# Kernel tuning notes

Measured on AMD Instinct MI355X. Metric: run time of the kernel, lower is better.

## Reference

```python
import jax, jax.numpy as jnp
import numpy as np

N, E, G = 50000, 800000, 512
C = 128          # in_channels = hidden_out_channel = out_channel
K = 3            # Chebyshev order (nb_filters)
NUM_EMB = 119    # largest OGB atom feature cardinality (padded common table)
EPS = 1e-5


def setup_inputs() -> dict:
    key = jax.random.key(0)
    ks = jax.random.split(key, 12)
    s = 0.05
    return {
        "atom_emb": jax.random.normal(ks[0], (9, NUM_EMB, C), jnp.float32) * s,
        "W1": jax.random.normal(ks[1], (K, C, C), jnp.float32) * s,
        "b1": jnp.zeros((C,), jnp.float32),
        "W3": jax.random.normal(ks[2], (K, C, C), jnp.float32) * s,
        "b3": jnp.zeros((C,), jnp.float32),
        "gamma": jnp.ones((C,), jnp.float32),
        "beta": jnp.zeros((C,), jnp.float32),
        "lw1": jax.random.normal(ks[3], (C, 16), jnp.float32) * s,
        "lb1": jnp.zeros((16,), jnp.float32),
        "lw2": jax.random.normal(ks[4], (16, 2), jnp.float32) * s,
        "lb2": jnp.zeros((2,), jnp.float32),
        "x": jax.random.randint(ks[5], (N, 9), 0, 2),
        "edge_index": jax.random.randint(ks[6], (2, E), 0, N),
        "batch": jnp.sort(jax.random.randint(ks[7], (N,), 0, G)),
    }


def _cheb_conv(h, row, col, norm, W, b):
    # PyG ChebConv, sym norm, lambda_max=2 => Lhat = -D^{-1/2} A D^{-1/2} (zero diag)
    def Lhat(z):
        return jax.ops.segment_sum(norm[:, None] * z[col], row, num_segments=N)
    Tx1 = Lhat(h)                      # T_1 = Lhat x
    Tx2 = 2.0 * Lhat(Tx1) - h          # T_2 = 2 Lhat T_1 - T_0
    return h @ W[0] + Tx1 @ W[1] + Tx2 @ W[2] + b


def reference(atom_emb, W1, b1, W3, b3, gamma, beta, lw1, lb1, lw2, lb2,
              x, edge_index, batch):
    row, col = edge_index[0], edge_index[1]
    # symmetric normalization weights (deg computed on row, as in get_laplacian)
    deg = jax.ops.segment_sum(jnp.ones((E,), jnp.float32), row, num_segments=N)
    dis = jnp.where(deg > 0, jax.lax.rsqrt(jnp.maximum(deg, 1.0)), 0.0)
    norm = -(dis[row] * dis[col])      # [E]

    # AtomEncoder: sum of 9 per-feature embeddings -> [N, C]
    h = atom_emb[jnp.arange(9), x].sum(axis=1)

    h = jax.nn.relu(_cheb_conv(h, row, col, norm, W1, b1))   # conv1
    h = jax.nn.relu(_cheb_conv(h, row, col, norm, W3, b3))   # conv3 (conv2 unused)

    # BatchNorm over nodes (training-mode batch stats, biased var)
    mu = h.mean(axis=0)
    var = jnp.mean((h - mu) ** 2, axis=0)
    h = (h - mu) * jax.lax.rsqrt(var + EPS) * gamma + beta

    # global_mean_pool over graphs
    sums = jax.ops.segment_sum(h, batch, num_segments=G)
    cnt = jax.ops.segment_sum(jnp.ones((N,), jnp.float32), batch, num_segments=G)
    pooled = sums / jnp.maximum(cnt, 1.0)[:, None]           # [G, C]

    out = jax.nn.relu(pooled @ lw1 + lb1) @ lw2 + lb2        # [G, 2]
    return out
```

## Files before the change

kernel.cpp:

```cpp
#include <hip/hip_runtime.h>
#include <hip/hip_bf16.h>

typedef __hip_bfloat16 bf16;
#define BN_EPS 1e-5f

typedef __attribute__((ext_vector_type(8))) short bf16x8;
typedef __attribute__((ext_vector_type(4))) float f32x4;

__device__ __forceinline__ float b2f(bf16 v){ return __bfloat162float(v); }
__device__ __forceinline__ float bu2f(unsigned short u){
  union { unsigned int i; float f; } x; x.i = ((unsigned int)u) << 16; return x.f;
}
__device__ __forceinline__ unsigned short f2bu(float f){
  bf16 b = __float2bfloat16(f);
  union { bf16 b; unsigned short u; } x; x.b = b; return x.u;
}
__device__ __forceinline__ float ldw(const void* p, size_t i, int wf){
  return wf ? ((const float*)p)[i] : b2f(((const bf16*)p)[i]);
}
__device__ __forceinline__ void up2(unsigned int w, float& lo, float& hi){
  union { unsigned int i; float f; } L, H;
  L.i = w << 16; H.i = w & 0xffff0000u;
  lo = L.f; hi = H.f;
}

__global__ void k_zero(int* __restrict__ p, int n,
                       const unsigned int* __restrict__ gbits, int* __restrict__ flag){
  int i = blockIdx.x * blockDim.x + threadIdx.x;
  if (i == 0) *flag = (gbits[0] == 0x3F800000u) ? 1 : 0;
  if (i < n) p[i] = 0;
}

__global__ __launch_bounds__(256) void k_bhist(const int* __restrict__ row, int E,
                                               int* __restrict__ gcnt){
  __shared__ int hist[256];
  int t = threadIdx.x;
  hist[t] = 0;
  __syncthreads();
  int base = blockIdx.x * 4096;
  #pragma unroll
  for (int j = 0; j < 16; ++j){
    int e = base + (j << 8) + t;
    if (e < E) atomicAdd(&hist[row[e] >> 8], 1);
  }
  __syncthreads();
  int h = hist[t];
  if (h > 0) atomicAdd(&gcnt[t], h);
}

__global__ __launch_bounds__(256) void k_bbase(const int* __restrict__ gcnt,
    int* __restrict__ bucketBase, int* __restrict__ gcur, int* __restrict__ rp, int N){
  __shared__ int ss[256];
  int t = threadIdx.x;
  int v = gcnt[t];
  ss[t] = v; __syncthreads();
  for (int o = 1; o < 256; o <<= 1){
    int u = (t >= o) ? ss[t - o] : 0;
    __syncthreads();
    ss[t] += u;
    __syncthreads();
  }
  int ex = ss[t] - v;
  bucketBase[t] = ex;
  gcur[t] = ex;
  if (t == 255){ bucketBase[256] = ss[255]; rp[N] = ss[255]; }
}

__global__ __launch_bounds__(256) void k_prep(int N,
    const void* __restrict__ Wa, unsigned short* __restrict__ WTa,
    const void* __restrict__ Wb, unsigned short* __restrict__ WTb,
    const void* __restrict__ emb, const int* __restrict__ x, int NE,
    unsigned short* __restrict__ h, const int* __restrict__ flag){
  int b = blockIdx.x;
  int t = threadIdx.x;
  int wf = *flag;
  if (b < 384){
    int id = b * 256 + t;
    const void* W = (id < 49152) ? Wa : Wb;
    unsigned short* WT = (id < 49152) ? WTa : WTb;
    int i = (id < 49152) ? id : id - 49152;
    int r = i >> 7, n = i & 127;
    float v;
    if (r < 128)       v = ldw(W, (size_t)r * 128 + n, wf)
                         - ldw(W, ((size_t)(256 + r)) * 128 + n, wf);
    else if (r < 256)  v = ldw(W, (size_t)r * 128 + n, wf);
    else               v = 2.f * ldw(W, (size_t)r * 128 + n, wf);
    WT[(size_t)n * 384 + r] = f2bu(v);
    return;
  }
  int gid = (b - 384) * 256 + t;
  int n = gid >> 4, c8 = (gid & 15) << 3;
  if (n >= N) return;
  float s[8];
  #pragma unroll
  for (int j = 0; j < 8; ++j) s[j] = 0.f;
  #pragma unroll
  for (int f = 0; f < 9; ++f){
    int idx = x[n * 9 + f];
    size_t base = ((size_t)(f * NE + idx) << 7) + c8;
    if (wf){
      const float* ep = (const float*)emb + base;
      #pragma unroll
      for (int j = 0; j < 8; ++j) s[j] += ep[j];
    } else {
      uint4 v = *(const uint4*)((const unsigned short*)emb + base);
      float lo, hi;
      up2(v.x, lo, hi); s[0] += lo; s[1] += hi;
      up2(v.y, lo, hi); s[2] += lo; s[3] += hi;
      up2(v.z, lo, hi); s[4] += lo; s[5] += hi;
      up2(v.w, lo, hi); s[6] += lo; s[7] += hi;
    }
  }
  uint4 r;
  r.x = ((unsigned int)f2bu(s[1]) << 16) | f2bu(s[0]);
  r.y = ((unsigned int)f2bu(s[3]) << 16) | f2bu(s[2]);
  r.z = ((unsigned int)f2bu(s[5]) << 16) | f2bu(s[4]);
  r.w = ((unsigned int)f2bu(s[7]) << 16) | f2bu(s[6]);
  *(uint4*)(h + ((size_t)n << 7) + c8) = r;
}

__global__ __launch_bounds__(256) void k_bfill1(const int* __restrict__ row,
    const int* __restrict__ col, int E,
    int* __restrict__ gcur, unsigned int* __restrict__ ebuf){
  __shared__ int hist[256];
  __shared__ int curs[256];
  int t = threadIdx.x;
  hist[t] = 0;
  __syncthreads();
  int base = blockIdx.x * 4096;
  int r[16], c[16];
  #pragma unroll
  for (int j = 0; j < 16; ++j){
    int e = base + (j << 8) + t;
    if (e < E){
      r[j] = row[e]; c[j] = col[e];
      atomicAdd(&hist[r[j] >> 8], 1);
    } else r[j] = -1;
  }
  __syncthreads();
  int h = hist[t];
  if (h > 0) curs[t] = atomicAdd(&gcur[t], h);
  __syncthreads();
  #pragma unroll
  for (int j = 0; j < 16; ++j){
    if (r[j] >= 0){
      int p = atomicAdd(&curs[r[j] >> 8], 1);
      ebuf[p] = ((unsigned int)c[j] << 8) | ((unsigned int)r[j] & 255u);
    }
  }
}

__global__ __launch_bounds__(256) void k_bfill2a(const unsigned int* __restrict__ ebuf,
    const int* __restrict__ bucketBase, int N,
    int* __restrict__ rp, float* __restrict__ dis){
  __shared__ int cnt[256];
  __shared__ int ss[256];
  int b = blockIdx.x, t = threadIdx.x;
  cnt[t] = 0;
  __syncthreads();
  int beg = bucketBase[b], end = bucketBase[b + 1];
  for (int p = beg + t; p < end; p += 256)
    atomicAdd(&cnt[ebuf[p] & 255u], 1);
  __syncthreads();
  int v = cnt[t];
  ss[t] = v; __syncthreads();
  for (int o = 1; o < 256; o <<= 1){
    int u = (t >= o) ? ss[t - o] : 0;
    __syncthreads();
    ss[t] += u;
    __syncthreads();
  }
  int idx = (b << 8) + t;
  if (idx < N){
    rp[idx] = beg + ss[t] - v;
    dis[idx] = (v > 0) ? rsqrtf((float)v) : 0.f;
  }
}

__global__ __launch_bounds__(256) void k_bfill2b(const unsigned int* __restrict__ ebuf,
    const int* __restrict__ bucketBase, const int* __restrict__ rp, int N,
    const float* __restrict__ dis, int2* __restrict__ cpack){
  __shared__ int lcur[256];
  __shared__ float sdis[256];
  int b = blockIdx.x, t = threadIdx.x;
  int idx = (b << 8) + t;
  lcur[t] = (idx < N) ? rp[idx] : 0;
  sdis[t] = (idx < N) ? dis[idx] : 0.f;
  __syncthreads();
  int beg = bucketBase[b], end = bucketBase[b + 1];
  for (int p = beg + t; p < end; p += 256){
    unsigned int pw = ebuf[p];
    int c = (int)(pw >> 8);
    int rl = (int)(pw & 255u);
    float nm = -(sdis[rl] * dis[c]);
    int slot = atomicAdd(&lcur[rl], 1);
    cpack[slot] = make_int2(c, __float_as_int(nm));
  }
}

__global__ __launch_bounds__(256) void k_spmm(const unsigned short* __restrict__ in,
    const int* __restrict__ rp, const int2* __restrict__ cpack,
    unsigned short* __restrict__ out, int N){
  int w = (blockIdx.x * 256 + threadIdx.x) >> 6;
  if (w >= N) return;
  int lane = threadIdx.x & 63;
  int quad = lane >> 4, ql = lane & 15;
  int p1 = rp[w + 1];
  int p = rp[w] + quad;
  const unsigned short* inq = in + (ql << 3);
  float a0 = 0.f, a1 = 0.f, a2 = 0.f, a3 = 0.f;
  float a4 = 0.f, a5 = 0.f, a6 = 0.f, a7 = 0.f;
  for (; p + 4 < p1; p += 8){
    int2 e0 = cpack[p];
    int2 e1 = cpack[p + 4];
    uint4 v0 = *(const uint4*)(inq + ((size_t)e0.x << 7));
    uint4 v1 = *(const uint4*)(inq + ((size_t)e1.x << 7));
    float w0 = __int_as_float(e0.y);
    float w1 = __int_as_float(e1.y);
    float lo, hi;
    up2(v0.x, lo, hi); a0 += w0 * lo; a1 += w0 * hi;
    up2(v0.y, lo, hi); a2 += w0 * lo; a3 += w0 * hi;
    up2(v0.z, lo, hi); a4 += w0 * lo; a5 += w0 * hi;
    up2(v0.w, lo, hi); a6 += w0 * lo; a7 += w0 * hi;
    up2(v1.x, lo, hi); a0 += w1 * lo; a1 += w1 * hi;
    up2(v1.y, lo, hi); a2 += w1 * lo; a3 += w1 * hi;
    up2(v1.z, lo, hi); a4 += w1 * lo; a5 += w1 * hi;
    up2(v1.w, lo, hi); a6 += w1 * lo; a7 += w1 * hi;
  }
  if (p < p1){
    int2 e0 = cpack[p];
    uint4 v0 = *(const uint4*)(inq + ((size_t)e0.x << 7));
    float w0 = __int_as_float(e0.y);
    float lo, hi;
    up2(v0.x, lo, hi); a0 += w0 * lo; a1 += w0 * hi;
    up2(v0.y, lo, hi); a2 += w0 * lo; a3 += w0 * hi;
    up2(v0.z, lo, hi); a4 += w0 * lo; a5 += w0 * hi;
    up2(v0.w, lo, hi); a6 += w0 * lo; a7 += w0 * hi;
  }
  a0 += __shfl_xor(a0, 16); a0 += __shfl_xor(a0, 32);
  a1 += __shfl_xor(a1, 16); a1 += __shfl_xor(a1, 32);
  a2 += __shfl_xor(a2, 16); a2 += __shfl_xor(a2, 32);
  a3 += __shfl_xor(a3, 16); a3 += __shfl_xor(a3, 32);
  a4 += __shfl_xor(a4, 16); a4 += __shfl_xor(a4, 32);
  a5 += __shfl_xor(a5, 16); a5 += __shfl_xor(a5, 32);
  a6 += __shfl_xor(a6, 16); a6 += __shfl_xor(a6, 32);
  a7 += __shfl_xor(a7, 16); a7 += __shfl_xor(a7, 32);
  if (quad == 0){
    uint4 r;
    r.x = ((unsigned int)f2bu(a1) << 16) | f2bu(a0);
    r.y = ((unsigned int)f2bu(a3) << 16) | f2bu(a2);
    r.z = ((unsigned int)f2bu(a5) << 16) | f2bu(a4);
    r.w = ((unsigned int)f2bu(a7) << 16) | f2bu(a6);
    *(uint4*)(out + ((size_t)w << 7) + (ql << 3)) = r;
  }
}

__global__ __launch_bounds__(256) void k_conv(const unsigned short* __restrict__ X,
    const unsigned short* __restrict__ T1, const unsigned short* __restrict__ T2,
    const unsigned short* __restrict__ WT,
    const void* __restrict__ bias,
    unsigned short* __restrict__ Y, int N, const int* __restrict__ flag,
    float* __restrict__ bns){
  int wf = *flag;
  __shared__ unsigned short As[128 * 40];
  __shared__ unsigned short Ws[128 * 40];
  int t = threadIdx.x;
  int wv = t >> 6, lane = t & 63;
  int m16 = lane & 15, quad = lane >> 4;
  int n0 = blockIdx.x * 128;

  f32x4 acc[2][8];
  #pragma unroll
  for (int i = 0; i < 2; ++i)
    #pragma unroll
    for (int j = 0; j < 8; ++j) acc[i][j] = (f32x4){0.f, 0.f, 0.f, 0.f};

  for (int kc = 0; kc < 12; ++kc){
    const unsigned short* src = (kc < 4) ? X : ((kc < 8) ? T1 : T2);
    int koff = (kc & 3) << 5;
    int kg = kc << 5;
    #pragma unroll
    for (int i = 0; i < 2; ++i){
      int id = t + (i << 8);
      int r = id >> 2, ks = id & 3;
      int node = n0 + r;
      uint4 v = make_uint4(0, 0, 0, 0);
      if (node < N) v = *(const uint4*)(src + ((size_t)node << 7) + koff + (ks << 3));
      *(uint4*)((void*)(As + r * 40 + (ks << 3))) = v;
    }
    #pragma unroll
    for (int i = 0; i < 2; ++i){
      int id = t + (i << 8);
      int n = id >> 2, ks = id & 3;
      uint4 v = *(const uint4*)(WT + (size_t)n * 384 + kg + (ks << 3));
      *(uint4*)((void*)(Ws + n * 40 + (ks << 3))) = v;
    }
    __syncthreads();
    bf16x8 af[2];
    af[0] = *(const bf16x8*)((const void*)(As + (32 * wv + m16) * 40 + (quad << 3)));
    af[1] = *(const bf16x8*)((const void*)(As + (32 * wv + 16 + m16) * 40 + (quad << 3)));
    #pragma unroll
    for (int tn = 0; tn < 8; ++tn){
      bf16x8 bf_ = *(const bf16x8*)((const void*)(Ws + (16 * tn + m16) * 40 + (quad << 3)));
      acc[0][tn] = __builtin_amdgcn_mfma_f32_16x16x32_bf16(af[0], bf_, acc[0][tn], 0, 0, 0);
      acc[1][tn] = __builtin_amdgcn_mfma_f32_16x16x32_bf16(af[1], bf_, acc[1][tn], 0, 0, 0);
    }
    __syncthreads();
  }
  float bv[8];
  #pragma unroll
  for (int tn = 0; tn < 8; ++tn) bv[tn] = ldw(bias, 16 * tn + m16, wf);
  float ps[8], pq[8];
  #pragma unroll
  for (int tn = 0; tn < 8; ++tn){ ps[tn] = 0.f; pq[tn] = 0.f; }
  #pragma unroll
  for (int ri = 0; ri < 2; ++ri){
    #pragma unroll
    for (int r = 0; r < 4; ++r){
      int node = n0 + 32 * wv + 16 * ri + quad * 4 + r;
      if (node < N){
        #pragma unroll
        for (int tn = 0; tn < 8; ++tn){
          float v = fmaxf(acc[ri][tn][r] + bv[tn], 0.f);
          Y[((size_t)node << 7) + 16 * tn + m16] = f2bu(v);
          ps[tn] += v; pq[tn] += v * v;
        }
      }
    }
  }
  if (bns){
    float* redf = (float*)As;
    int rg = (wv << 2) | quad;
    #pragma unroll
    for (int tn = 0; tn < 8; ++tn) redf[rg * 128 + tn * 16 + m16] = ps[tn];
    __syncthreads();
    if (t < 128){
      float a = 0.f;
      #pragma unroll
      for (int r = 0; r < 16; ++r) a += redf[r * 128 + t];
      atomicAdd(&bns[t], a);
    }
    __syncthreads();
    #pragma unroll
    for (int tn = 0; tn < 8; ++tn) redf[rg * 128 + tn * 16 + m16] = pq[tn];
    __syncthreads();
    if (t < 128){
      float a = 0.f;
      #pragma unroll
      for (int r = 0; r < 16; ++r) a += redf[r * 128 + t];
      atomicAdd(&bns[128 + t], a);
    }
  }
}

__device__ __forceinline__ int lbound(const int* a, int n, int key){
  int lo = 0, hi = n;
  while (lo < hi){ int mid = (lo + hi) >> 1; if (a[mid] < key) lo = mid + 1; else hi = mid; }
  return lo;
}

__global__ __launch_bounds__(128) void k_pool(const unsigned short* __restrict__ h,
    const int* __restrict__ batchv, int N, const float* __restrict__ bns,
    const void* __restrict__ gamma, const void* __restrict__ beta,
    const void* __restrict__ lw1, const void* __restrict__ lb1,
    const void* __restrict__ lw2, const void* __restrict__ lb2,
    void* __restrict__ out, const int* __restrict__ flag){
  int wf = *flag;
  int g = blockIdx.x;
  int t = threadIdx.x;
  int c8 = (t & 15) << 3;
  int rg = t >> 4;
  __shared__ int slo, shi;
  if (t == 0){ slo = lbound(batchv, N, g); shi = lbound(batchv, N, g + 1); }
  __syncthreads();
  int lo = slo, hi = shi, cnt = hi - lo;
  float s[8];
  #pragma unroll
  for (int j = 0; j < 8; ++j) s[j] = 0.f;
  for (int n = lo + rg; n < hi; n += 8){
    uint4 v = *(const uint4*)(h + ((size_t)n << 7) + c8);
    float a, b;
    up2(v.x, a, b); s[0] += a; s[1] += b;
    up2(v.y, a, b); s[2] += a; s[3] += b;
    up2(v.z, a, b); s[4] += a; s[5] += b;
    up2(v.w, a, b); s[6] += a; s[7] += b;
  }
  __shared__ float red[8][128];
  *(float4*)(&red[rg][c8])     = (float4){s[0], s[1], s[2], s[3]};
  *(float4*)(&red[rg][c8 + 4]) = (float4){s[4], s[5], s[6], s[7]};
  __syncthreads();
  int c = t;
  float acc = 0.f;
  #pragma unroll
  for (int r = 0; r < 8; ++r) acc += red[r][c];
  float pooled = acc / (float)(cnt > 0 ? cnt : 1);
  float mu = bns[c] / (float)N;
  float var = bns[128 + c] / (float)N - mu * mu;
  float sc = ldw(gamma, c, wf) * rsqrtf(var + BN_EPS);
  float sh = ldw(beta, c, wf) - mu * sc;
  float pb = (cnt > 0) ? (pooled * sc + sh) : 0.f;
  __shared__ float sp[128];
  __shared__ float hid[16];
  sp[c] = pb; __syncthreads();
  if (c < 16){
    float sm = ldw(lb1, c, wf);
    for (int i = 0; i < 128; ++i) sm += sp[i] * ldw(lw1, i * 16 + c, wf);
    hid[c] = fmaxf(sm, 0.f);
  }
  __syncthreads();
  if (c < 2){
    float sm = ldw(lb2, c, wf);
    for (int j = 0; j < 16; ++j) sm += hid[j] * ldw(lw2, j * 2 + c, wf);
    if (wf) ((float*)out)[g * 2 + c] = sm;
    else    ((bf16*)out)[g * 2 + c] = __float2bfloat16(sm);
  }
}

extern "C" void kernel_launch(void* const* d_in, const int* in_sizes, int n_in,
                              void* d_out, int out_size, void* d_ws, size_t ws_size,
                              hipStream_t stream){
  const void* emb   = d_in[0];
  const void* W1    = d_in[1];
  const void* b1    = d_in[2];
  const void* W3    = d_in[3];
  const void* b3    = d_in[4];
  const void* gamma = d_in[5];
  const void* beta  = d_in[6];
  const void* lw1   = d_in[7];
  const void* lb1   = d_in[8];
  const void* lw2   = d_in[9];
  const void* lb2   = d_in[10];
  const int* x      = (const int*)d_in[11];
  const int* ei     = (const int*)d_in[12];
  const int* batchv = (const int*)d_in[13];
  (void)n_in; (void)ws_size;

  int N  = in_sizes[13];
  int E  = in_sizes[12] / 2;
  int NE = in_sizes[0] / (9 * 128);
  int G  = out_size / 2;
  const int* row = ei;
  const int* col = ei + E;

  char* ws = (char*)d_ws;
  size_t off = 0;
  auto alloc = [&](size_t bytes) -> char* {
    char* p = ws + off;
    off += (bytes + 255) & ~(size_t)255;
    return p;
  };
  int*   flag = (int*)alloc(4);
  int*   gcnt = (int*)alloc(256 * 4);
  float* bns  = (float*)alloc(256 * 4);
  int*   bucketBase = (int*)alloc(257 * 4);
  int*   gcur = (int*)alloc(256 * 4);
  int*   rp   = (int*)alloc((size_t)(N + 1) * 4);
  float* dis  = (float*)alloc((size_t)N * 4);
  unsigned int* ebuf = (unsigned int*)alloc((size_t)E * 4);
  int2*  cpack = (int2*)alloc((size_t)E * 8);
  unsigned short* wt1 = (unsigned short*)alloc(49152 * 2);
  unsigned short* wt2 = (unsigned short*)alloc(49152 * 2);
  size_t fb = ((size_t)N * 128 * 2 + 255) & ~(size_t)255;
  unsigned short* Hf = (unsigned short*)alloc(fb);
  unsigned short* Tf = (unsigned short*)alloc(fb);
  unsigned short* Zf = (unsigned short*)alloc(fb);

  k_zero<<<2, 256, 0, stream>>>(gcnt, 512, (const unsigned int*)gamma, flag);

  int ebk = (E + 4095) / 4096;
  int NB  = (N + 255) / 256;
  k_bhist<<<ebk, 256, 0, stream>>>(row, E, gcnt);
  k_bbase<<<1, 256, 0, stream>>>(gcnt, bucketBase, gcur, rp, N);
  int pb = 384 + (int)(((size_t)N * 16 + 255) / 256);
  k_prep<<<pb, 256, 0, stream>>>(N, W1, wt1, W3, wt2, emb, x, NE, Hf, flag);
  k_bfill1<<<ebk, 256, 0, stream>>>(row, col, E, gcur, ebuf);
  k_bfill2a<<<NB, 256, 0, stream>>>(ebuf, bucketBase, N, rp, dis);
  k_bfill2b<<<NB, 256, 0, stream>>>(ebuf, bucketBase, rp, N, dis, cpack);

  int sb = (N + 3) / 4;
  int cb = (N + 127) / 128;
  k_spmm<<<sb, 256, 0, stream>>>(Hf, rp, cpack, Tf, N);
  k_spmm<<<sb, 256, 0, stream>>>(Tf, rp, cpack, Zf, N);
  k_conv<<<cb, 256, 0, stream>>>(Hf, Tf, Zf, wt1, b1, Hf, N, flag, nullptr);
  k_spmm<<<sb, 256, 0, stream>>>(Hf, rp, cpack, Tf, N);
  k_spmm<<<sb, 256, 0, stream>>>(Tf, rp, cpack, Zf, N);
  k_conv<<<cb, 256, 0, stream>>>(Hf, Tf, Zf, wt2, b3, Hf, N, flag, bns);

  k_pool<<<G, 128, 0, stream>>>(Hf, batchv, N, bns, gamma, beta, lw1, lb1, lw2, lb2,
                                d_out, flag);
}
```

Measured before the change: 320.2 us.

## Fuse CSR build and prep kernels into one persistent kernel with grid barriers

Merges six preprocessing launches (bucket histogram, bucket scan, prep, bucket fill, per-row count, packed-edge fill) into a single persistent 256-block kernel. The dependent phases are separated by software grid barriers built on an atomic counter, so launch gaps and tail effects between the small kernels go away. The SpMM inner loop is also unrolled from 2 to 4 gathers per quad to put more loads in flight. The spin barrier relies on all 256 blocks being resident at once, and it serialises phases that previously ran as separate kernels.

```diff
diff --git a/kernel.cpp b/kernel.cpp
--- a/kernel.cpp
+++ b/kernel.cpp
@@ -3,6 +3,7 @@
 
 typedef __hip_bfloat16 bf16;
 #define BN_EPS 1e-5f
+#define NBLK 256
 
 typedef __attribute__((ext_vector_type(8))) short bf16x8;
 typedef __attribute__((ext_vector_type(4))) float f32x4;
@@ -22,6 +23,17 @@
   union { unsigned int i; float f; } L, H;
   L.i = w << 16; H.i = w & 0xffff0000u;
   lo = L.f; hi = H.f;
+}
+
+__device__ __forceinline__ void gbar(int* cnt, int target){
+  __threadfence();
+  __syncthreads();
+  if (threadIdx.x == 0){
+    atomicAdd(cnt, 1);
+    while (atomicAdd(cnt, 0) < target) {}
+  }
+  __syncthreads();
+  __threadfence();
 }
 
 __global__ void k_zero(int* __restrict__ p, int n,
@@ -31,170 +43,165 @@
   if (i < n) p[i] = 0;
 }
 
-__global__ __launch_bounds__(256) void k_bhist(const int* __restrict__ row, int E,
-                                               int* __restrict__ gcnt){
-  __shared__ int hist[256];
-  int t = threadIdx.x;
-  hist[t] = 0;
-  __syncthreads();
-  int base = blockIdx.x * 4096;
-  #pragma unroll
-  for (int j = 0; j < 16; ++j){
-    int e = base + (j << 8) + t;
-    if (e < E) atomicAdd(&hist[row[e] >> 8], 1);
-  }
-  __syncthreads();
-  int h = hist[t];
-  if (h > 0) atomicAdd(&gcnt[t], h);
-}
-
-__global__ __launch_bounds__(256) void k_bbase(const int* __restrict__ gcnt,
-    int* __restrict__ bucketBase, int* __restrict__ gcur, int* __restrict__ rp, int N){
-  __shared__ int ss[256];
-  int t = threadIdx.x;
-  int v = gcnt[t];
-  ss[t] = v; __syncthreads();
-  for (int o = 1; o < 256; o <<= 1){
-    int u = (t >= o) ? ss[t - o] : 0;
-    __syncthreads();
-    ss[t] += u;
-    __syncthreads();
-  }
-  int ex = ss[t] - v;
-  bucketBase[t] = ex;
-  gcur[t] = ex;
-  if (t == 255){ bucketBase[256] = ss[255]; rp[N] = ss[255]; }
-}
-
-__global__ __launch_bounds__(256) void k_prep(int N,
+__global__ __launch_bounds__(256) void k_pre(
+    const int* __restrict__ row, const int* __restrict__ col, int E, int N, int NE,
+    int* __restrict__ gcnt, int* __restrict__ gcur,
+    int* __restrict__ rp, float* __restrict__ dis,
+    unsigned int* __restrict__ ebuf, int2* __restrict__ cpack,
+    int* __restrict__ bar,
     const void* __restrict__ Wa, unsigned short* __restrict__ WTa,
     const void* __restrict__ Wb, unsigned short* __restrict__ WTb,
-    const void* __restrict__ emb, const int* __restrict__ x, int NE,
+    const void* __restrict__ emb, const int* __restrict__ x,
     unsigned short* __restrict__ h, const int* __restrict__ flag){
-  int b = blockIdx.x;
-  int t = threadIdx.x;
+  __shared__ int sbase[257];
+  __shared__ int sA[256];
+  __shared__ int sB[256];
+  __shared__ float sF[256];
+  int t = threadIdx.x, b = blockIdx.x;
+
+  sA[t] = 0;
+  __syncthreads();
+  for (int e = b * 256 + t; e < E; e += NBLK * 256)
+    atomicAdd(&sA[row[e] >> 8], 1);
+  __syncthreads();
+  if (sA[t] > 0) atomicAdd(&gcnt[t], sA[t]);
+  gbar(bar, NBLK);
+
+  {
+    int v = gcnt[t];
+    sB[t] = v;
+    __syncthreads();
+    for (int o = 1; o < 256; o <<= 1){
+      int u = (t >= o) ? sB[t - o] : 0;
+      __syncthreads();
+      sB[t] += u;
+      __syncthreads();
+    }
+    sbase[t] = sB[t] - v;
+    if (t == 255) sbase[256] = sB[255];
+    if (b == 0){
+      gcur[t] = sB[t] - v;
+      if (t == 255) rp[N] = sB[255];
+    }
+    __syncthreads();
+  }
+  gbar(bar, NBLK * 2);
+
+  for (int base = b * 4096; base < E; base += NBLK * 4096){
+    sA[t] = 0;
+    __syncthreads();
+    int r[16], c[16];
+    #pragma unroll
+    for (int j = 0; j < 16; ++j){
+      int e = base + (j << 8) + t;
+      if (e < E){
+        r[j] = row[e]; c[j] = col[e];
+        atomicAdd(&sA[r[j] >> 8], 1);
+      } else r[j] = -1;
+    }
+    __syncthreads();
+    int hh = sA[t];
+    if (hh > 0) sB[t] = atomicAdd(&gcur[t], hh);
+    __syncthreads();
+    #pragma unroll
+    for (int j = 0; j < 16; ++j){
+      if (r[j] >= 0){
+        int pp = atomicAdd(&sB[r[j] >> 8], 1);
+        ebuf[pp] = ((unsigned int)c[j] << 8) | ((unsigned int)r[j] & 255u);
+      }
+    }
+    __syncthreads();
+  }
+  gbar(bar, NBLK * 3);
+
+  int NB = (N + 255) >> 8;
+  for (int bk = b; bk < NB; bk += NBLK){
+    sA[t] = 0;
+    __syncthreads();
+    int beg = sbase[bk], end = sbase[bk + 1];
+    for (int p = beg + t; p < end; p += 256)
+      atomicAdd(&sA[ebuf[p] & 255u], 1);
+    __syncthreads();
+    int vv = sA[t];
+    sB[t] = vv;
+    __syncthreads();
+    for (int o = 1; o < 256; o <<= 1){
+      int u = (t >= o) ? sB[t - o] : 0;
+      __syncthreads();
+      sB[t] += u;
+      __syncthreads();
+    }
+    int idx = (bk << 8) + t;
+    if (idx < N){
+      rp[idx] = beg + sB[t] - vv;
+      dis[idx] = (vv > 0) ? rsqrtf((float)vv) : 0.f;
+    }
+    __syncthreads();
+  }
+  gbar(bar, NBLK * 4);
+
+  for (int bk = b; bk < NB; bk += NBLK){
+    int idx = (bk << 8) + t;
+    sA[t] = (idx < N) ? rp[idx] : 0;
+    sF[t] = (idx < N) ? dis[idx] : 0.f;
+    __syncthreads();
+    int beg = sbase[bk], end = sbase[bk + 1];
+    for (int p = beg + t; p < end; p += 256){
+      unsigned int pw = ebuf[p];
+      int cc = (int)(pw >> 8);
+      int rl = (int)(pw & 255u);
+      float nm = -(sF[rl] * dis[cc]);
+      int slot = atomicAdd(&sA[rl], 1);
+      cpack[slot] = make_int2(cc, __float_as_int(nm));
+    }
+    __syncthreads();
+  }
+
   int wf = *flag;
-  if (b < 384){
-    int id = b * 256 + t;
-    const void* W = (id < 49152) ? Wa : Wb;
-    unsigned short* WT = (id < 49152) ? WTa : WTb;
-    int i = (id < 49152) ? id : id - 49152;
-    int r = i >> 7, n = i & 127;
-    float v;
-    if (r < 128)       v = ldw(W, (size_t)r * 128 + n, wf)
-                         - ldw(W, ((size_t)(256 + r)) * 128 + n, wf);
-    else if (r < 256)  v = ldw(W, (size_t)r * 128 + n, wf);
-    else               v = 2.f * ldw(W, (size_t)r * 128 + n, wf);
-    WT[(size_t)n * 384 + r] = f2bu(v);
-    return;
-  }
-  int gid = (b - 384) * 256 + t;
-  int n = gid >> 4, c8 = (gid & 15) << 3;
-  if (n >= N) return;
-  float s[8];
-  #pragma unroll
-  for (int j = 0; j < 8; ++j) s[j] = 0.f;
-  #pragma unroll
-  for (int f = 0; f < 9; ++f){
-    int idx = x[n * 9 + f];
-    size_t base = ((size_t)(f * NE + idx) << 7) + c8;
-    if (wf){
-      const float* ep = (const float*)emb + base;
+  long long total = 98304LL + (long long)N * 16;
+  for (long long id = (long long)b * 256 + t; id < total; id += (long long)NBLK * 256){
+    if (id < 98304){
+      int iid = (int)id;
+      const void* W = (iid < 49152) ? Wa : Wb;
+      unsigned short* WT = (iid < 49152) ? WTa : WTb;
+      int i = (iid < 49152) ? iid : iid - 49152;
+      int r = i >> 7, n = i & 127;
+      float v;
+      if (r < 128)       v = ldw(W, (size_t)r * 128 + n, wf)
+                           - ldw(W, ((size_t)(256 + r)) * 128 + n, wf);
+      else if (r < 256)  v = ldw(W, (size_t)r * 128 + n, wf);
+      else               v = 2.f * ldw(W, (size_t)r * 128 + n, wf);
+      WT[(size_t)n * 384 + r] = f2bu(v);
+    } else {
+      long long gid = id - 98304;
+      int n = (int)(gid >> 4), c8 = ((int)gid & 15) << 3;
+      float s[8];
       #pragma unroll
-      for (int j = 0; j < 8; ++j) s[j] += ep[j];
-    } else {
-      uint4 v = *(const uint4*)((const unsigned short*)emb + base);
-      float lo, hi;
-      up2(v.x, lo, hi); s[0] += lo; s[1] += hi;
-      up2(v.y, lo, hi); s[2] += lo; s[3] += hi;
-      up2(v.z, lo, hi); s[4] += lo; s[5] += hi;
-      up2(v.w, lo, hi); s[6] += lo; s[7] += hi;
-    }
-  }
-  uint4 r;
-  r.x = ((unsigned int)f2bu(s[1]) << 16) | f2bu(s[0]);
-  r.y = ((unsigned int)f2bu(s[3]) << 16) | f2bu(s[2]);
-  r.z = ((unsigned int)f2bu(s[5]) << 16) | f2bu(s[4]);
-  r.w = ((unsigned int)f2bu(s[7]) << 16) | f2bu(s[6]);
-  *(uint4*)(h + ((size_t)n << 7) + c8) = r;
-}
-
-__global__ __launch_bounds__(256) void k_bfill1(const int* __restrict__ row,
-    const int* __restrict__ col, int E,
-    int* __restrict__ gcur, unsigned int* __restrict__ ebuf){
-  __shared__ int hist[256];
-  __shared__ int curs[256];
-  int t = threadIdx.x;
-  hist[t] = 0;
-  __syncthreads();
-  int base = blockIdx.x * 4096;
-  int r[16], c[16];
-  #pragma unroll
-  for (int j = 0; j < 16; ++j){
-    int e = base + (j << 8) + t;
-    if (e < E){
-      r[j] = row[e]; c[j] = col[e];
-      atomicAdd(&hist[r[j] >> 8], 1);
-    } else r[j] = -1;
-  }
-  __syncthreads();
-  int h = hist[t];
-  if (h > 0) curs[t] = atomicAdd(&gcur[t], h);
-  __syncthreads();
-  #pragma unroll
-  for (int j = 0; j < 16; ++j){
-    if (r[j] >= 0){
-      int p = atomicAdd(&curs[r[j] >> 8], 1);
-      ebuf[p] = ((unsigned int)c[j] << 8) | ((unsigned int)r[j] & 255u);
-    }
-  }
-}
-
-__global__ __launch_bounds__(256) void k_bfill2a(const unsigned int* __restrict__ ebuf,
-    const int* __restrict__ bucketBase, int N,
-    int* __restrict__ rp, float* __restrict__ dis){
-  __shared__ int cnt[256];
-  __shared__ int ss[256];
-  int b = blockIdx.x, t = threadIdx.x;
-  cnt[t] = 0;
-  __syncthreads();
-  int beg = bucketBase[b], end = bucketBase[b + 1];
-  for (int p = beg + t; p < end; p += 256)
-    atomicAdd(&cnt[ebuf[p] & 255u], 1);
-  __syncthreads();
-  int v = cnt[t];
-  ss[t] = v; __syncthreads();
-  for (int o = 1; o < 256; o <<= 1){
-    int u = (t >= o) ? ss[t - o] : 0;
-    __syncthreads();
-    ss[t] += u;
-    __syncthreads();
-  }
-  int idx = (b << 8) + t;
-  if (idx < N){
-    rp[idx] = beg + ss[t] - v;
-    dis[idx] = (v > 0) ? rsqrtf((float)v) : 0.f;
-  }
-}
-
-__global__ __launch_bounds__(256) void k_bfill2b(const unsigned int* __restrict__ ebuf,
-    const int* __restrict__ bucketBase, const int* __restrict__ rp, int N,
-    const float* __restrict__ dis, int2* __restrict__ cpack){
-  __shared__ int lcur[256];
-  __shared__ float sdis[256];
-  int b = blockIdx.x, t = threadIdx.x;
-  int idx = (b << 8) + t;
-  lcur[t] = (idx < N) ? rp[idx] : 0;
-  sdis[t] = (idx < N) ? dis[idx] : 0.f;
-  __syncthreads();
-  int beg = bucketBase[b], end = bucketBase[b + 1];
-  for (int p = beg + t; p < end; p += 256){
-    unsigned int pw = ebuf[p];
-    int c = (int)(pw >> 8);
-    int rl = (int)(pw & 255u);
-    float nm = -(sdis[rl] * dis[c]);
-    int slot = atomicAdd(&lcur[rl], 1);
-    cpack[slot] = make_int2(c, __float_as_int(nm));
+      for (int j = 0; j < 8; ++j) s[j] = 0.f;
+      #pragma unroll
+      for (int f = 0; f < 9; ++f){
+        int idx = x[n * 9 + f];
+        size_t bs = ((size_t)(f * NE + idx) << 7) + c8;
+        if (wf){
+          const float* ep = (const float*)emb + bs;
+          #pragma unroll
+          for (int j = 0; j < 8; ++j) s[j] += ep[j];
+        } else {
+          uint4 v = *(const uint4*)((const unsigned short*)emb + bs);
+          float lo, hi;
+          up2(v.x, lo, hi); s[0] += lo; s[1] += hi;
+          up2(v.y, lo, hi); s[2] += lo; s[3] += hi;
+          up2(v.z, lo, hi); s[4] += lo; s[5] += hi;
+          up2(v.w, lo, hi); s[6] += lo; s[7] += hi;
+        }
+      }
+      uint4 r;
+      r.x = ((unsigned int)f2bu(s[1]) << 16) | f2bu(s[0]);
+      r.y = ((unsigned int)f2bu(s[3]) << 16) | f2bu(s[2]);
+      r.z = ((unsigned int)f2bu(s[5]) << 16) | f2bu(s[4]);
+      r.w = ((unsigned int)f2bu(s[7]) << 16) | f2bu(s[6]);
+      *(uint4*)(h + ((size_t)n << 7) + c8) = r;
+    }
   }
 }
 
@@ -210,33 +217,33 @@
   const unsigned short* inq = in + (ql << 3);
   float a0 = 0.f, a1 = 0.f, a2 = 0.f, a3 = 0.f;
   float a4 = 0.f, a5 = 0.f, a6 = 0.f, a7 = 0.f;
-  for (; p + 4 < p1; p += 8){
+#define ACC(V, W) { float lo, hi; \
+    up2(V.x, lo, hi); a0 += (W) * lo; a1 += (W) * hi; \
+    up2(V.y, lo, hi); a2 += (W) * lo; a3 += (W) * hi; \
+    up2(V.z, lo, hi); a4 += (W) * lo; a5 += (W) * hi; \
+    up2(V.w, lo, hi); a6 += (W) * lo; a7 += (W) * hi; }
+  for (; p + 12 < p1; p += 16){
     int2 e0 = cpack[p];
     int2 e1 = cpack[p + 4];
+    int2 e2 = cpack[p + 8];
+    int2 e3 = cpack[p + 12];
     uint4 v0 = *(const uint4*)(inq + ((size_t)e0.x << 7));
     uint4 v1 = *(const uint4*)(inq + ((size_t)e1.x << 7));
+    uint4 v2 = *(const uint4*)(inq + ((size_t)e2.x << 7));
+    uint4 v3 = *(const uint4*)(inq + ((size_t)e3.x << 7));
     float w0 = __int_as_float(e0.y);
     float w1 = __int_as_float(e1.y);
-    float lo, hi;
-    up2(v0.x, lo, hi); a0 += w0 * lo; a1 += w0 * hi;
-    up2(v0.y, lo, hi); a2 += w0 * lo; a3 += w0 * hi;
-    up2(v0.z, lo, hi); a4 += w0 * lo; a5 += w0 * hi;
-    up2(v0.w, lo, hi); a6 += w0 * lo; a7 += w0 * hi;
-    up2(v1.x, lo, hi); a0 += w1 * lo; a1 += w1 * hi;
-    up2(v1.y, lo, hi); a2 += w1 * lo; a3 += w1 * hi;
-    up2(v1.z, lo, hi); a4 += w1 * lo; a5 += w1 * hi;
-    up2(v1.w, lo, hi); a6 += w1 * lo; a7 += w1 * hi;
-  }
-  if (p < p1){
+    float w2 = __int_as_float(e2.y);
+    float w3 = __int_as_float(e3.y);
+    ACC(v0, w0); ACC(v1, w1); ACC(v2, w2); ACC(v3, w3);
+  }
+  for (; p < p1; p += 4){
     int2 e0 = cpack[p];
     uint4 v0 = *(const uint4*)(inq + ((size_t)e0.x << 7));
     float w0 = __int_as_float(e0.y);
-    float lo, hi;
-    up2(v0.x, lo, hi); a0 += w0 * lo; a1 += w0 * hi;
-    up2(v0.y, lo, hi); a2 += w0 * lo; a3 += w0 * hi;
-    up2(v0.z, lo, hi); a4 += w0 * lo; a5 += w0 * hi;
-    up2(v0.w, lo, hi); a6 += w0 * lo; a7 += w0 * hi;
-  }
+    ACC(v0, w0);
+  }
+#undef ACC
   a0 += __shfl_xor(a0, 16); a0 += __shfl_xor(a0, 32);
   a1 += __shfl_xor(a1, 16); a1 += __shfl_xor(a1, 32);
   a2 += __shfl_xor(a2, 16); a2 += __shfl_xor(a2, 32);
@@ -452,7 +459,7 @@
   int*   flag = (int*)alloc(4);
   int*   gcnt = (int*)alloc(256 * 4);
   float* bns  = (float*)alloc(256 * 4);
-  int*   bucketBase = (int*)alloc(257 * 4);
+  int*   bar  = (int*)alloc(64 * 4);
   int*   gcur = (int*)alloc(256 * 4);
   int*   rp   = (int*)alloc((size_t)(N + 1) * 4);
   float* dis  = (float*)alloc((size_t)N * 4);
@@ -465,17 +472,11 @@
   unsigned short* Tf = (unsigned short*)alloc(fb);
   unsigned short* Zf = (unsigned short*)alloc(fb);
 
-  k_zero<<<2, 256, 0, stream>>>(gcnt, 512, (const unsigned int*)gamma, flag);
-
-  int ebk = (E + 4095) / 4096;
-  int NB  = (N + 255) / 256;
-  k_bhist<<<ebk, 256, 0, stream>>>(row, E, gcnt);
-  k_bbase<<<1, 256, 0, stream>>>(gcnt, bucketBase, gcur, rp, N);
-  int pb = 384 + (int)(((size_t)N * 16 + 255) / 256);
-  k_prep<<<pb, 256, 0, stream>>>(N, W1, wt1, W3, wt2, emb, x, NE, Hf, flag);
-  k_bfill1<<<ebk, 256, 0, stream>>>(row, col, E, gcur, ebuf);
-  k_bfill2a<<<NB, 256, 0, stream>>>(ebuf, bucketBase, N, rp, dis);
-  k_bfill2b<<<NB, 256, 0, stream>>>(ebuf, bucketBase, rp, N, dis, cpack);
+  k_zero<<<3, 256, 0, stream>>>(gcnt, 576, (const unsigned int*)gamma, flag);
+
+  k_pre<<<NBLK, 256, 0, stream>>>(row, col, E, N, NE,
+                                  gcnt, gcur, rp, dis, ebuf, cpack, bar,
+                                  W1, wt1, W3, wt2, emb, x, Hf, flag);
 
   int sb = (N + 3) / 4;
   int cb = (N + 127) / 128;
```

After: 496.0 us. 1.55x slower.
